# Optimization experiments

Hardware: AMD Instinct MI355X
Metric: run time of the kernel (lower is better)

The kernel has to match this reference:

```python
import jax, jax.numpy as jnp
import numpy as np

N_MESH = 40962  # icosahedral level-6 mesh nodes (x[..., -40962:])


def _lin_coords(out_size, in_size, scale):
    # torch F.interpolate bilinear, align_corners=False source coords
    i = jnp.arange(out_size, dtype=jnp.float32)
    src = jnp.maximum((i + 0.5) / scale - 0.5, 0.0)
    i0 = jnp.clip(jnp.floor(src).astype(jnp.int32), 0, in_size - 1)
    i1 = jnp.minimum(i0 + 1, in_size - 1)
    w = src - i0.astype(jnp.float32)
    return i0, i1, w


def _bilinear4(x):
    # x: (B,C,H,W) -> (B,C,4H,4W), separable bilinear, align_corners=False
    B, C, H, W = x.shape
    i0, i1, wh = _lin_coords(4 * H, H, 4.0)
    x = x[:, :, i0, :] * (1.0 - wh)[None, None, :, None] + x[:, :, i1, :] * wh[None, None, :, None]
    j0, j1, ww = _lin_coords(4 * W, W, 4.0)
    x = x[:, :, :, j0] * (1.0 - ww) + x[:, :, :, j1] * ww
    return x


def _grid2mesh(x, lat, lon):
    # x: (B,C,H,W); drop last lat row, upsample x4, append broadcast pole row
    B, C, H, W = x.shape
    pole = x[:, :, -1, 0][:, :, None, None] * jnp.ones((B, C, 1, 4 * W), x.dtype)
    xi = _bilinear4(x[:, :, :-1, :])            # (B,C,4(H-1),4W)
    xi = jnp.concatenate([xi, pole], axis=2)    # (B,C,4(H-1)+1,4W)
    return xi[:, :, lat - 1, lon - 1]           # (B,C,M) gather at mesh coords


def _gcn(h, W, b, src, dst, norm, n):
    # GCNConv: sym-normalized scatter-add aggregation of linearly transformed feats
    h = h @ W                                    # (B,N,Hd)
    msg = lambda hb: jax.ops.segment_sum(hb[src] * norm[:, None], dst, num_segments=n)
    return jax.vmap(msg)(h) + b


def reference(x, edge_index, Lat, Lon, W1, b1, W2, b2, Wl, bl, Wl1, bl1):
    B, C, H, Wd = x.shape
    mesh = _grid2mesh(x, Lat, Lon)                               # (B,C,M)
    feats = jnp.concatenate([x.reshape(B, C, H * Wd), mesh], -1)  # (B,C,N)
    h = feats.transpose(0, 2, 1)                                 # (B,N,C)
    n = h.shape[1]

    # gcn_norm with self loops (edge_weight = 1)
    loops = jnp.arange(n, dtype=edge_index.dtype)
    src = jnp.concatenate([edge_index[0], loops])
    dst = jnp.concatenate([edge_index[1], loops])
    deg = jax.ops.segment_sum(jnp.ones(src.shape, h.dtype), dst, num_segments=n)
    dinv = jnp.where(deg > 0, deg ** -0.5, 0.0)
    norm = dinv[src] * dinv[dst]

    h = _gcn(h, W1, b1, src, dst, norm, n)
    h = jax.nn.gelu(h, approximate=False)
    h = _gcn(h, W2, b2, src, dst, norm, n)
    h = h[:, -N_MESH:, :]                                        # keep mesh nodes
    out = jax.nn.gelu((h @ Wl + bl) @ Wl1 + bl1, approximate=False)
    return out.transpose(0, 2, 1)                                # (B,out_ch,M)


def setup_inputs() -> dict:
    key = jax.random.key(0)
    ks = jax.random.split(key, 16)
    B, C, H, W = 1, 69, 181, 360
    HID, OUT = 256, 256
    N = H * W + N_MESH  # 106122
    E = 500000
    x = jax.random.normal(ks[0], (B, C, H, W), jnp.float32)
    edge_index = jax.random.randint(ks[1], (2, E), 0, N, dtype=jnp.int64)
    Lat = jax.random.randint(ks[2], (N_MESH,), 1, 4 * (H - 1) + 2, dtype=jnp.int64)
    Lon = jax.random.randint(ks[3], (N_MESH,), 1, 4 * W + 1, dtype=jnp.int64)
    s = 0.05
    return {
        "x": x, "edge_index": edge_index, "Lat": Lat, "Lon": Lon,
        "W1": jax.random.normal(ks[4], (C, HID), jnp.float32) * s,
        "b1": jnp.zeros((HID,), jnp.float32),
        "W2": jax.random.normal(ks[5], (HID, HID), jnp.float32) * s,
        "b2": jnp.zeros((HID,), jnp.float32),
        "Wl": jax.random.normal(ks[6], (HID, 256), jnp.float32) * s,
        "bl": jnp.zeros((256,), jnp.float32),
        "Wl1": jax.random.normal(ks[7], (256, OUT), jnp.float32) * s,
        "bl1": jnp.zeros((OUT,), jnp.float32),
    }
```

## Files before the change

kernel.cpp:

```cpp
#include <hip/hip_runtime.h>

#define NGRID 65160
#define NMESH 40962
#define NTOT  (NGRID + NMESH)
#define CIN   69
#define KPAD1 96
#define HID   256
#define HH    181
#define WWID  360
#define SCAN_BS 1024
#define NBLK_SCAN ((NTOT + SCAN_BS - 1) / SCAN_BS)

#define NT1TILES ((NTOT + 63) / 64)
#define NT1PAD   (NT1TILES * 64)
#define NT2TILES ((NMESH + 63) / 64)
#define NT2PAD   (NT2TILES * 64)

#define W1OFF  0
#define WCOFF  (96 * 256)
#define WALLK  (96 + 256)

typedef float f32x4 __attribute__((ext_vector_type(4)));
typedef _Float16 f16;
typedef _Float16 f16x2 __attribute__((ext_vector_type(2)));
typedef _Float16 f16x4 __attribute__((ext_vector_type(4)));
typedef _Float16 f16x8 __attribute__((ext_vector_type(8)));

__device__ __forceinline__ float gelu_exact(float v) {
    return 0.5f * v * (1.0f + erff(v * 0.7071067811865476f));
}

__global__ __launch_bounds__(256) void transpose_x(const float* __restrict__ x,
                                                   f16* __restrict__ h0g) {
    __shared__ float tile[96][65];
    int s0 = blockIdx.x * 64;
    int t = threadIdx.x;
#pragma unroll
    for (int i = 0; i < 24; ++i) {
        int idx = t + i * 256;
        int c = idx >> 6, s = idx & 63;
        int gs = s0 + s;
        float v = 0.f;
        if (c < CIN && gs < NGRID) v = x[(size_t)c * NGRID + gs];
        tile[c][s] = v;
    }
    __syncthreads();
#pragma unroll
    for (int i = 0; i < 12; ++i) {
        int idx = t + i * 256;
        int r = idx / 48, u = idx % 48;
        int gr = s0 + r;
        if (gr < NGRID) {
            f16x2 p;
            p.x = (f16)tile[u * 2 + 0][r];
            p.y = (f16)tile[u * 2 + 1][r];
            ((f16x2*)h0g)[(size_t)gr * 48 + u] = p;
        }
    }
}

__global__ __launch_bounds__(256) void mesh_interp(const f16* __restrict__ h0g,
                                                   const int* __restrict__ Lat,
                                                   const int* __restrict__ Lon,
                                                   f16* __restrict__ h0m) {
    int t = blockIdx.x * 256 + threadIdx.x;
    if (t >= NMESH * 48) return;
    int j = t / 48, u = t % 48;
    int la = Lat[j] - 1;
    int lo = Lon[j] - 1;
    const f16x2* g = (const f16x2*)h0g;
    f16x2 o;
    if (la == 720) {
        o = g[(size_t)(180 * WWID) * 48 + u];
    } else {
        float sh = fmaxf((la + 0.5f) * 0.25f - 0.5f, 0.0f);
        int i0 = min((int)sh, HH - 2);
        int i1 = min(i0 + 1, HH - 2);
        float wh = sh - (float)i0;
        float sw = fmaxf((lo + 0.5f) * 0.25f - 0.5f, 0.0f);
        int j0 = min((int)sw, WWID - 1);
        int j1 = min(j0 + 1, WWID - 1);
        float ww = sw - (float)j0;
        f16x2 v00 = g[(size_t)(i0 * WWID + j0) * 48 + u];
        f16x2 v10 = g[(size_t)(i1 * WWID + j0) * 48 + u];
        f16x2 v01 = g[(size_t)(i0 * WWID + j1) * 48 + u];
        f16x2 v11 = g[(size_t)(i1 * WWID + j1) * 48 + u];
        float ax = (float)v00.x + ((float)v10.x - (float)v00.x) * wh;
        float ay = (float)v00.y + ((float)v10.y - (float)v00.y) * wh;
        float bx = (float)v01.x + ((float)v11.x - (float)v01.x) * wh;
        float by = (float)v01.y + ((float)v11.y - (float)v01.y) * wh;
        o.x = (f16)(ax + (bx - ax) * ww);
        o.y = (f16)(ay + (by - ay) * ww);
    }
    ((f16x2*)h0m)[(size_t)j * 48 + u] = o;
}

__global__ void deg_init(float* __restrict__ deg, int* __restrict__ cnt) {
    int i = blockIdx.x * 256 + threadIdx.x;
    if (i < NTOT) { deg[i] = 1.0f; cnt[i] = 0; }
}
__global__ void deg_scatter(const int* __restrict__ ei, float* __restrict__ deg, int E) {
    int e = blockIdx.x * 256 + threadIdx.x;
    if (e < E) atomicAdd(&deg[ei[E + e]], 1.0f);
}

__global__ __launch_bounds__(SCAN_BS) void scan1(const float* __restrict__ deg,
                                                 float* __restrict__ dinv,
                                                 int* __restrict__ off, int* __restrict__ bsum) {
    __shared__ int s[SCAN_BS];
    int t = threadIdx.x;
    int i = blockIdx.x * SCAN_BS + t;
    int v = (i < NTOT) ? ((int)deg[i] - 1) : 0;
    if (i < NTOT) dinv[i] = 1.0f / sqrtf((float)(v + 1));
    s[t] = v; __syncthreads();
    for (int d = 1; d < SCAN_BS; d <<= 1) {
        int x = (t >= d) ? s[t - d] : 0;
        __syncthreads();
        s[t] += x;
        __syncthreads();
    }
    if (i < NTOT) off[i] = s[t] - v;
    if (t == SCAN_BS - 1) bsum[blockIdx.x] = s[t];
}
__global__ void scan2(int* __restrict__ bsum) {
    __shared__ int s[128];
    int t = threadIdx.x;
    int v = (t < NBLK_SCAN) ? bsum[t] : 0;
    s[t] = v; __syncthreads();
    for (int d = 1; d < 128; d <<= 1) {
        int x = (t >= d) ? s[t - d] : 0;
        __syncthreads();
        s[t] += x;
        __syncthreads();
    }
    if (t < NBLK_SCAN) bsum[t] = s[t] - v;
}
__global__ __launch_bounds__(SCAN_BS) void scan3(int* __restrict__ off, const int* __restrict__ bsum) {
    int i = blockIdx.x * SCAN_BS + threadIdx.x;
    if (i < NTOT) off[i] += bsum[blockIdx.x];
}

__global__ void csr_fill(const int* __restrict__ ei, const float* __restrict__ dinv,
                         const int* __restrict__ off, int* __restrict__ cnt,
                         int2* __restrict__ epk, int E) {
    int e = blockIdx.x * 256 + threadIdx.x;
    if (e >= E) return;
    int s = ei[e], d = ei[E + e];
    int pos = off[d] + atomicAdd(&cnt[d], 1);
    epk[pos] = make_int2(s, __float_as_int(dinv[s] * dinv[d]));
}

__global__ __launch_bounds__(256) void wgemm(const float* __restrict__ A,
                                             const float* __restrict__ B,
                                             float* __restrict__ C) {
    __shared__ float As[16][68];
    __shared__ float Bs[16][64];
    int r0 = blockIdx.y * 64, c0 = blockIdx.x * 64;
    int t = threadIdx.x;
    int tr = t >> 4, tc = t & 15;
    float acc[4][4] = {};
    for (int kk = 0; kk < 256; kk += 16) {
#pragma unroll
        for (int i = 0; i < 4; ++i) {
            int idx = t + i * 256;
            int r = idx >> 4, k = idx & 15;
            As[k][r] = A[(size_t)(r0 + r) * 256 + kk + k];
        }
#pragma unroll
        for (int i = 0; i < 4; ++i) {
            int idx = t + i * 256;
            int k = idx >> 6, c = idx & 63;
            Bs[k][c] = B[(size_t)(kk + k) * 256 + c0 + c];
        }
        __syncthreads();
#pragma unroll
        for (int k = 0; k < 16; ++k) {
            float a[4], b[4];
#pragma unroll
            for (int i = 0; i < 4; ++i) a[i] = As[k][tr * 4 + i];
#pragma unroll
            for (int j = 0; j < 4; ++j) b[j] = Bs[k][tc * 4 + j];
#pragma unroll
            for (int i = 0; i < 4; ++i)
#pragma unroll
                for (int j = 0; j < 4; ++j) acc[i][j] = fmaf(a[i], b[j], acc[i][j]);
        }
        __syncthreads();
    }
#pragma unroll
    for (int i = 0; i < 4; ++i)
#pragma unroll
        for (int j = 0; j < 4; ++j)
            C[(size_t)(r0 + tr * 4 + i) * 256 + c0 + tc * 4 + j] = acc[i][j];
}

__global__ __launch_bounds__(256) void bias_k(const float* __restrict__ b2,
                                              const float* __restrict__ M1,
                                              const float* __restrict__ bl,
                                              const float* __restrict__ Wl1,
                                              const float* __restrict__ bl1,
                                              float* __restrict__ bc) {
    int c = threadIdx.x;
    float acc = bl1[c];
    for (int j = 0; j < 256; ++j) {
        acc = fmaf(b2[j], M1[(size_t)j * 256 + c], acc);
        acc = fmaf(bl[j], Wl1[(size_t)j * 256 + c], acc);
    }
    bc[c] = acc;
}

__global__ void pack_f16(const float* __restrict__ W1, const float* __restrict__ Wc,
                         f16* __restrict__ wp) {
    int t = blockIdx.x * 256 + threadIdx.x;
    if (t >= WALLK * HID) return;
    int kg = t >> 8, c = t & 255;
    float v;
    size_t idx;
    if (kg < 96) {
        v = (kg < CIN) ? W1[(size_t)kg * HID + c] : 0.f;
        idx = W1OFF + ((((size_t)(kg >> 3)) * HID + c) << 3) + (kg & 7);
    } else {
        int ks = kg - 96;
        int kl = (ks & ~63) + ((ks & 3) << 4) + ((ks & 63) >> 2);
        v = Wc[(size_t)kl * HID + c];
        idx = WCOFF + ((((size_t)(ks >> 3)) * HID + c) << 3) + (ks & 7);
    }
    wp[idx] = (f16)v;
}

__global__ __launch_bounds__(256) void agg1(const f16* __restrict__ h0,
                                            const float* __restrict__ deg,
                                            const float* __restrict__ dinv,
                                            const int* __restrict__ off,
                                            const int2* __restrict__ epk,
                                            f16* __restrict__ P0) {
    int wv = (blockIdx.x * 256 + threadIdx.x) >> 6;
    if (wv >= NT1PAD) return;
    int lane = threadIdx.x & 63;
    if (lane >= 48) return;
    int r = wv & 63, tile = wv >> 6;
    char* dst = (char*)P0 + (size_t)tile * 12288 + ((r * 192 + lane * 4) ^ ((r & 7) << 4));
    if (wv >= NTOT) { *(unsigned*)dst = 0u; return; }
    int d = wv;
    const f16x2* g = (const f16x2*)h0;
    float dv = dinv[d];
    float w2 = dv * dv;
    f16x2 v = g[(size_t)d * 48 + lane];
    float ax = w2 * (float)v.x;
    float ay = w2 * (float)v.y;
    const int2* ep = epk + off[d];
    int n = (int)deg[d] - 1;
    int p = 0;
    for (; p + 4 <= n; p += 4) {
        int2 e0 = ep[p], e1 = ep[p + 1], e2 = ep[p + 2], e3 = ep[p + 3];
        f16x2 u0 = g[(size_t)e0.x * 48 + lane];
        f16x2 u1 = g[(size_t)e1.x * 48 + lane];
        f16x2 u2 = g[(size_t)e2.x * 48 + lane];
        f16x2 u3 = g[(size_t)e3.x * 48 + lane];
        float w0 = __int_as_float(e0.y), w1 = __int_as_float(e1.y);
        float w2b = __int_as_float(e2.y), w3 = __int_as_float(e3.y);
        ax = fmaf(w0, (float)u0.x, ax); ay = fmaf(w0, (float)u0.y, ay);
        ax = fmaf(w1, (float)u1.x, ax); ay = fmaf(w1, (float)u1.y, ay);
        ax = fmaf(w2b, (float)u2.x, ax); ay = fmaf(w2b, (float)u2.y, ay);
        ax = fmaf(w3, (float)u3.x, ax); ay = fmaf(w3, (float)u3.y, ay);
    }
    for (; p < n; ++p) {
        int2 e = ep[p];
        f16x2 u = g[(size_t)e.x * 48 + lane];
        float w = __int_as_float(e.y);
        ax = fmaf(w, (float)u.x, ax);
        ay = fmaf(w, (float)u.y, ay);
    }
    f16x2 o; o.x = (f16)ax; o.y = (f16)ay;
    *(f16x2*)dst = o;
}

__global__ __launch_bounds__(256) void agg2(const f16* __restrict__ A,
                                            const float* __restrict__ deg,
                                            const float* __restrict__ dinv,
                                            const int* __restrict__ off,
                                            const int2* __restrict__ epk,
                                            f16* __restrict__ P2) {
    int wv = (blockIdx.x * 256 + threadIdx.x) >> 6;
    if (wv >= NT2PAD) return;
    int lane = threadIdx.x & 63;
    int r = wv & 63, tile = wv >> 6;
    char* dst = (char*)P2 + (size_t)tile * 32768 + ((r * 512 + lane * 8) ^ ((r & 7) << 4));
    if (wv >= NMESH) { *(unsigned long long*)dst = 0ull; return; }
    int d = NGRID + wv;
    const f16x4* g = (const f16x4*)A;
    float dv = dinv[d];
    float w2 = dv * dv;
    f16x4 v = g[(size_t)d * 64 + lane];
    float4 acc;
    acc.x = w2 * (float)v.x; acc.y = w2 * (float)v.y;
    acc.z = w2 * (float)v.z; acc.w = w2 * (float)v.w;
    const int2* ep = epk + off[d];
    int n = (int)deg[d] - 1;
    int p = 0;
    for (; p + 4 <= n; p += 4) {
        int2 e0 = ep[p], e1 = ep[p + 1], e2 = ep[p + 2], e3 = ep[p + 3];
        f16x4 u0 = g[(size_t)e0.x * 64 + lane];
        f16x4 u1 = g[(size_t)e1.x * 64 + lane];
        f16x4 u2 = g[(size_t)e2.x * 64 + lane];
        f16x4 u3 = g[(size_t)e3.x * 64 + lane];
        float w0 = __int_as_float(e0.y), w1 = __int_as_float(e1.y);
        float w2b = __int_as_float(e2.y), w3 = __int_as_float(e3.y);
        acc.x = fmaf(w0, (float)u0.x, acc.x); acc.y = fmaf(w0, (float)u0.y, acc.y);
        acc.z = fmaf(w0, (float)u0.z, acc.z); acc.w = fmaf(w0, (float)u0.w, acc.w);
        acc.x = fmaf(w1, (float)u1.x, acc.x); acc.y = fmaf(w1, (float)u1.y, acc.y);
        acc.z = fmaf(w1, (float)u1.z, acc.z); acc.w = fmaf(w1, (float)u1.w, acc.w);
        acc.x = fmaf(w2b, (float)u2.x, acc.x); acc.y = fmaf(w2b, (float)u2.y, acc.y);
        acc.z = fmaf(w2b, (float)u2.z, acc.z); acc.w = fmaf(w2b, (float)u2.w, acc.w);
        acc.x = fmaf(w3, (float)u3.x, acc.x); acc.y = fmaf(w3, (float)u3.y, acc.y);
        acc.z = fmaf(w3, (float)u3.z, acc.z); acc.w = fmaf(w3, (float)u3.w, acc.w);
    }
    for (; p < n; ++p) {
        int2 e = ep[p];
        f16x4 u = g[(size_t)e.x * 64 + lane];
        float w = __int_as_float(e.y);
        acc.x = fmaf(w, (float)u.x, acc.x); acc.y = fmaf(w, (float)u.y, acc.y);
        acc.z = fmaf(w, (float)u.z, acc.z); acc.w = fmaf(w, (float)u.w, acc.w);
    }
    f16x4 o;
    o.x = (f16)acc.x; o.y = (f16)acc.y; o.z = (f16)acc.z; o.w = (f16)acc.w;
    *(f16x4*)dst = o;
}

__global__ __launch_bounds__(256) void gemm1_f16(const f16* __restrict__ P0,
                                                 const f16* __restrict__ wp,
                                                 const float* __restrict__ bias,
                                                 f16* __restrict__ Af) {
    __shared__ __align__(16) f16 As[64 * 96];
    const int tile = blockIdx.x;
    const int row0 = tile * 64;
    const int t = threadIdx.x;
    const int lane = t & 63;
    const int wave = t >> 6;
    const int l15 = lane & 15, l4 = lane >> 4;
    const int colw = wave * 64;
    const char* src = (const char*)P0 + (size_t)tile * 12288;
#pragma unroll
    for (int i = 0; i < 3; ++i) {
        int o = t * 16 + i * 4096;
        *(uint4*)((char*)As + o) = *(const uint4*)(src + o);
    }
    __syncthreads();
    f32x4 acc[4][4] = {};
#pragma unroll
    for (int ks = 0; ks < 96; ks += 32) {
        f16x8 a[4], b[4];
#pragma unroll
        for (int rb = 0; rb < 4; ++rb) {
            int r = rb * 16 + l15;
            int byte = r * 192 + (ks + l4 * 8) * 2;
            int swz = byte ^ ((r & 7) << 4);
            a[rb] = *(f16x8*)((char*)As + swz);
        }
#pragma unroll
        for (int cb = 0; cb < 4; ++cb) {
            int c = colw + cb * 16 + l15;
            size_t off = ((((size_t)ks >> 3) + l4) * HID + c) << 3;
            b[cb] = *(const f16x8*)(wp + W1OFF + off);
        }
#pragma unroll
        for (int rb = 0; rb < 4; ++rb)
#pragma unroll
            for (int cb = 0; cb < 4; ++cb)
                acc[rb][cb] = __builtin_amdgcn_mfma_f32_16x16x32_f16(a[rb], b[cb], acc[rb][cb], 0, 0, 0);
    }
#pragma unroll
    for (int rb = 0; rb < 4; ++rb) {
#pragma unroll
        for (int r = 0; r < 4; ++r) {
            int gr = row0 + rb * 16 + l4 * 4 + r;
            if (gr < NTOT) {
                f16x4 o;
#pragma unroll
                for (int cb = 0; cb < 4; ++cb) {
                    int gc = colw + cb * 16 + l15;
                    float v = acc[rb][cb][r] + bias[gc];
                    o[cb] = (f16)gelu_exact(v);
                }
                *(f16x4*)(Af + (size_t)gr * HID + colw + l15 * 4) = o;
            }
        }
    }
}

__global__ __launch_bounds__(256) void final_k(const f16* __restrict__ P2,
                                               const f16* __restrict__ wp,
                                               const float* __restrict__ bc,
                                               float* __restrict__ out) {
    __shared__ __align__(16) char smem[64 * 132 * 4];
    f16* Ps = (f16*)smem;
    float* lf = (float*)smem;
    const int tile = blockIdx.x;
    const int row0 = tile * 64;
    const int t = threadIdx.x;
    const int lane = t & 63;
    const int wave = t >> 6;
    const int l15 = lane & 15, l4 = lane >> 4;
    const int cw = wave * 64;
    const char* src = (const char*)P2 + (size_t)tile * 32768;
#pragma unroll
    for (int i = 0; i < 8; ++i) {
        int o = t * 16 + i * 4096;
        *(uint4*)((char*)Ps + o) = *(const uint4*)(src + o);
    }
    __syncthreads();
    f32x4 acc[4][4] = {};
#pragma unroll
    for (int ks = 0; ks < 256; ks += 32) {
        f16x8 w[4], p[4];
#pragma unroll
        for (int mb = 0; mb < 4; ++mb) {
            int c = cw + mb * 16 + l15;
            size_t off = ((((size_t)ks >> 3) + l4) * HID + c) << 3;
            w[mb] = *(const f16x8*)(wp + WCOFF + off);
        }
#pragma unroll
        for (int jb = 0; jb < 4; ++jb) {
            int r = jb * 16 + l15;
            int byte = r * 512 + (ks + l4 * 8) * 2;
            int swz = byte ^ ((r & 7) << 4);
            p[jb] = *(f16x8*)((char*)Ps + swz);
        }
#pragma unroll
        for (int mb = 0; mb < 4; ++mb)
#pragma unroll
            for (int jb = 0; jb < 4; ++jb)
                acc[mb][jb] = __builtin_amdgcn_mfma_f32_16x16x32_f16(w[mb], p[jb], acc[mb][jb], 0, 0, 0);
    }
    const bool full = (row0 + 64 <= NMESH);
    for (int ph = 0; ph < 2; ++ph) {
        __syncthreads();
        if ((wave >> 1) == ph) {
            int cbase = cw & 127;
#pragma unroll
            for (int mb = 0; mb < 4; ++mb) {
                int chl = cbase + mb * 16 + l4 * 4;
                int c = cw + mb * 16 + l4 * 4;
                float b0 = bc[c + 0], b1v = bc[c + 1], b2v = bc[c + 2], b3v = bc[c + 3];
#pragma unroll
                for (int jb = 0; jb < 4; ++jb) {
                    int j = jb * 16 + l15;
                    float4 o;
                    o.x = gelu_exact(acc[mb][jb][0] + b0);
                    o.y = gelu_exact(acc[mb][jb][1] + b1v);
                    o.z = gelu_exact(acc[mb][jb][2] + b2v);
                    o.w = gelu_exact(acc[mb][jb][3] + b3v);
                    *(float4*)&lf[j * 132 + chl] = o;
                }
            }
        }
        __syncthreads();
        if (full) {
#pragma unroll
            for (int i = 0; i < 8; ++i) {
                int id = t + i * 256;
                int chl = id >> 4, n0 = (id & 15) * 4;
                float4 v;
                v.x = lf[(n0 + 0) * 132 + chl];
                v.y = lf[(n0 + 1) * 132 + chl];
                v.z = lf[(n0 + 2) * 132 + chl];
                v.w = lf[(n0 + 3) * 132 + chl];
                *(float4*)(out + (size_t)(ph * 128 + chl) * NMESH + row0 + n0) = v;
            }
        } else {
            for (int i = 0; i < 8; ++i) {
                int id = t + i * 256;
                int chl = id >> 4, n0 = (id & 15) * 4;
                for (int k2 = 0; k2 < 4; ++k2)
                    if (row0 + n0 + k2 < NMESH)
                        out[(size_t)(ph * 128 + chl) * NMESH + row0 + n0 + k2] =
                            lf[(n0 + k2) * 132 + chl];
            }
        }
    }
}

extern "C" void kernel_launch(void* const* d_in, const int* in_sizes, int n_in,
                              void* d_out, int out_size, void* d_ws, size_t ws_size,
                              hipStream_t stream) {
    const float* x   = (const float*)d_in[0];
    const int*   ei  = (const int*)d_in[1];
    const int*   Lat = (const int*)d_in[2];
    const int*   Lon = (const int*)d_in[3];
    const float* W1  = (const float*)d_in[4];
    const float* b1  = (const float*)d_in[5];
    const float* W2  = (const float*)d_in[6];
    const float* b2  = (const float*)d_in[7];
    const float* Wl  = (const float*)d_in[8];
    const float* bl  = (const float*)d_in[9];
    const float* Wl1 = (const float*)d_in[10];
    const float* bl1 = (const float*)d_in[11];
    float* out = (float*)d_out;
    const int E = in_sizes[1] / 2;

    f16*   h0  = (f16*)d_out;
    int2*  epk = (int2*)((char*)d_out + (size_t)NTOT * KPAD1 * 2);

    f16*   P0   = (f16*)d_ws;
    f16*   Af   = P0 + (size_t)NT1TILES * 6144;
    f16*   P2   = Af + (size_t)NTOT * HID;
    float* deg  = (float*)(P2 + (size_t)NT2TILES * 16384);
    float* dinv = deg + NTOT;
    int*   off  = (int*)(dinv + NTOT);
    int*   cnt  = off + NTOT;
    int*   bsum = cnt + NTOT;
    float* M1   = (float*)(bsum + 128);
    float* WcF  = M1 + HID * HID;
    float* bc   = WcF + HID * HID;
    f16*   wp   = (f16*)(bc + HID);

    transpose_x<<<(NGRID + 63) / 64, 256, 0, stream>>>(x, h0);
    mesh_interp<<<(NMESH * 48 + 255) / 256, 256, 0, stream>>>(h0, Lat, Lon,
                                                              h0 + (size_t)NGRID * KPAD1);

    deg_init<<<(NTOT + 255) / 256, 256, 0, stream>>>(deg, cnt);
    deg_scatter<<<(E + 255) / 256, 256, 0, stream>>>(ei, deg, E);
    scan1<<<NBLK_SCAN, SCAN_BS, 0, stream>>>(deg, dinv, off, bsum);
    scan2<<<1, 128, 0, stream>>>(bsum);
    scan3<<<NBLK_SCAN, SCAN_BS, 0, stream>>>(off, bsum);
    csr_fill<<<(E + 255) / 256, 256, 0, stream>>>(ei, dinv, off, cnt, epk, E);

    dim3 gW(4, 4);
    wgemm<<<gW, 256, 0, stream>>>(Wl, Wl1, M1);
    wgemm<<<gW, 256, 0, stream>>>(W2, M1, WcF);
    bias_k<<<1, 256, 0, stream>>>(b2, M1, bl, Wl1, bl1, bc);
    pack_f16<<<(WALLK * HID + 255) / 256, 256, 0, stream>>>(W1, WcF, wp);

    agg1<<<(int)(((long long)NT1PAD * 64 + 255) / 256), 256, 0, stream>>>(
        h0, deg, dinv, off, epk, P0);
    gemm1_f16<<<NT1TILES, 256, 0, stream>>>(P0, wp, b1, Af);

    agg2<<<(int)(((long long)NT2PAD * 64 + 255) / 256), 256, 0, stream>>>(
        Af, deg, dinv, off, epk, P2);

    final_k<<<NT2TILES, 256, 0, stream>>>(P2, wp, bc, out);
}
```

Baseline: 271.7 us.

## Fuse neighbor aggregation into both GEMM kernels, dropping staged P buffers

The separate agg1/agg2 gather kernels are merged into the MFMA GEMM kernels. Each block now aggregates its 64 rows directly into shared memory, with each wave looping over 16 rows, before running the matmul. This removes the global round-trip of the swizzled P0/P2 intermediates and two kernel launches. The edge list moves from the output buffer to workspace, since fused2 now writes output while other blocks still read edges. The trade-off is far fewer concurrent waves issuing gathers, so there is less latency hiding for the irregular loads.

```diff
diff --git a/kernel.cpp b/kernel.cpp
--- a/kernel.cpp
+++ b/kernel.cpp
@@ -12,9 +12,7 @@
 #define NBLK_SCAN ((NTOT + SCAN_BS - 1) / SCAN_BS)
 
 #define NT1TILES ((NTOT + 63) / 64)
-#define NT1PAD   (NT1TILES * 64)
 #define NT2TILES ((NMESH + 63) / 64)
-#define NT2PAD   (NT2TILES * 64)
 
 #define W1OFF  0
 #define WCOFF  (96 * 256)
@@ -228,109 +226,14 @@
     wp[idx] = (f16)v;
 }
 
-__global__ __launch_bounds__(256) void agg1(const f16* __restrict__ h0,
-                                            const float* __restrict__ deg,
-                                            const float* __restrict__ dinv,
-                                            const int* __restrict__ off,
-                                            const int2* __restrict__ epk,
-                                            f16* __restrict__ P0) {
-    int wv = (blockIdx.x * 256 + threadIdx.x) >> 6;
-    if (wv >= NT1PAD) return;
-    int lane = threadIdx.x & 63;
-    if (lane >= 48) return;
-    int r = wv & 63, tile = wv >> 6;
-    char* dst = (char*)P0 + (size_t)tile * 12288 + ((r * 192 + lane * 4) ^ ((r & 7) << 4));
-    if (wv >= NTOT) { *(unsigned*)dst = 0u; return; }
-    int d = wv;
-    const f16x2* g = (const f16x2*)h0;
-    float dv = dinv[d];
-    float w2 = dv * dv;
-    f16x2 v = g[(size_t)d * 48 + lane];
-    float ax = w2 * (float)v.x;
-    float ay = w2 * (float)v.y;
-    const int2* ep = epk + off[d];
-    int n = (int)deg[d] - 1;
-    int p = 0;
-    for (; p + 4 <= n; p += 4) {
-        int2 e0 = ep[p], e1 = ep[p + 1], e2 = ep[p + 2], e3 = ep[p + 3];
-        f16x2 u0 = g[(size_t)e0.x * 48 + lane];
-        f16x2 u1 = g[(size_t)e1.x * 48 + lane];
-        f16x2 u2 = g[(size_t)e2.x * 48 + lane];
-        f16x2 u3 = g[(size_t)e3.x * 48 + lane];
-        float w0 = __int_as_float(e0.y), w1 = __int_as_float(e1.y);
-        float w2b = __int_as_float(e2.y), w3 = __int_as_float(e3.y);
-        ax = fmaf(w0, (float)u0.x, ax); ay = fmaf(w0, (float)u0.y, ay);
-        ax = fmaf(w1, (float)u1.x, ax); ay = fmaf(w1, (float)u1.y, ay);
-        ax = fmaf(w2b, (float)u2.x, ax); ay = fmaf(w2b, (float)u2.y, ay);
-        ax = fmaf(w3, (float)u3.x, ax); ay = fmaf(w3, (float)u3.y, ay);
-    }
-    for (; p < n; ++p) {
-        int2 e = ep[p];
-        f16x2 u = g[(size_t)e.x * 48 + lane];
-        float w = __int_as_float(e.y);
-        ax = fmaf(w, (float)u.x, ax);
-        ay = fmaf(w, (float)u.y, ay);
-    }
-    f16x2 o; o.x = (f16)ax; o.y = (f16)ay;
-    *(f16x2*)dst = o;
-}
-
-__global__ __launch_bounds__(256) void agg2(const f16* __restrict__ A,
-                                            const float* __restrict__ deg,
-                                            const float* __restrict__ dinv,
-                                            const int* __restrict__ off,
-                                            const int2* __restrict__ epk,
-                                            f16* __restrict__ P2) {
-    int wv = (blockIdx.x * 256 + threadIdx.x) >> 6;
-    if (wv >= NT2PAD) return;
-    int lane = threadIdx.x & 63;
-    int r = wv & 63, tile = wv >> 6;
-    char* dst = (char*)P2 + (size_t)tile * 32768 + ((r * 512 + lane * 8) ^ ((r & 7) << 4));
-    if (wv >= NMESH) { *(unsigned long long*)dst = 0ull; return; }
-    int d = NGRID + wv;
-    const f16x4* g = (const f16x4*)A;
-    float dv = dinv[d];
-    float w2 = dv * dv;
-    f16x4 v = g[(size_t)d * 64 + lane];
-    float4 acc;
-    acc.x = w2 * (float)v.x; acc.y = w2 * (float)v.y;
-    acc.z = w2 * (float)v.z; acc.w = w2 * (float)v.w;
-    const int2* ep = epk + off[d];
-    int n = (int)deg[d] - 1;
-    int p = 0;
-    for (; p + 4 <= n; p += 4) {
-        int2 e0 = ep[p], e1 = ep[p + 1], e2 = ep[p + 2], e3 = ep[p + 3];
-        f16x4 u0 = g[(size_t)e0.x * 64 + lane];
-        f16x4 u1 = g[(size_t)e1.x * 64 + lane];
-        f16x4 u2 = g[(size_t)e2.x * 64 + lane];
-        f16x4 u3 = g[(size_t)e3.x * 64 + lane];
-        float w0 = __int_as_float(e0.y), w1 = __int_as_float(e1.y);
-        float w2b = __int_as_float(e2.y), w3 = __int_as_float(e3.y);
-        acc.x = fmaf(w0, (float)u0.x, acc.x); acc.y = fmaf(w0, (float)u0.y, acc.y);
-        acc.z = fmaf(w0, (float)u0.z, acc.z); acc.w = fmaf(w0, (float)u0.w, acc.w);
-        acc.x = fmaf(w1, (float)u1.x, acc.x); acc.y = fmaf(w1, (float)u1.y, acc.y);
-        acc.z = fmaf(w1, (float)u1.z, acc.z); acc.w = fmaf(w1, (float)u1.w, acc.w);
-        acc.x = fmaf(w2b, (float)u2.x, acc.x); acc.y = fmaf(w2b, (float)u2.y, acc.y);
-        acc.z = fmaf(w2b, (float)u2.z, acc.z); acc.w = fmaf(w2b, (float)u2.w, acc.w);
-        acc.x = fmaf(w3, (float)u3.x, acc.x); acc.y = fmaf(w3, (float)u3.y, acc.y);
-        acc.z = fmaf(w3, (float)u3.z, acc.z); acc.w = fmaf(w3, (float)u3.w, acc.w);
-    }
-    for (; p < n; ++p) {
-        int2 e = ep[p];
-        f16x4 u = g[(size_t)e.x * 64 + lane];
-        float w = __int_as_float(e.y);
-        acc.x = fmaf(w, (float)u.x, acc.x); acc.y = fmaf(w, (float)u.y, acc.y);
-        acc.z = fmaf(w, (float)u.z, acc.z); acc.w = fmaf(w, (float)u.w, acc.w);
-    }
-    f16x4 o;
-    o.x = (f16)acc.x; o.y = (f16)acc.y; o.z = (f16)acc.z; o.w = (f16)acc.w;
-    *(f16x4*)dst = o;
-}
-
-__global__ __launch_bounds__(256) void gemm1_f16(const f16* __restrict__ P0,
-                                                 const f16* __restrict__ wp,
-                                                 const float* __restrict__ bias,
-                                                 f16* __restrict__ Af) {
+__global__ __launch_bounds__(256) void fused1(const f16* __restrict__ h0,
+                                              const float* __restrict__ deg,
+                                              const float* __restrict__ dinv,
+                                              const int* __restrict__ off,
+                                              const int2* __restrict__ epk,
+                                              const f16* __restrict__ wp,
+                                              const float* __restrict__ bias,
+                                              f16* __restrict__ Af) {
     __shared__ __align__(16) f16 As[64 * 96];
     const int tile = blockIdx.x;
     const int row0 = tile * 64;
@@ -339,13 +242,48 @@
     const int wave = t >> 6;
     const int l15 = lane & 15, l4 = lane >> 4;
     const int colw = wave * 64;
-    const char* src = (const char*)P0 + (size_t)tile * 12288;
-#pragma unroll
-    for (int i = 0; i < 3; ++i) {
-        int o = t * 16 + i * 4096;
-        *(uint4*)((char*)As + o) = *(const uint4*)(src + o);
+
+    if (lane < 48) {
+        const f16x2* g = (const f16x2*)h0;
+        for (int i = 0; i < 16; ++i) {
+            int r = wave * 16 + i;
+            int d = row0 + r;
+            char* dst = (char*)As + ((r * 192 + lane * 4) ^ ((r & 7) << 4));
+            if (d >= NTOT) { *(unsigned*)dst = 0u; continue; }
+            float dv = dinv[d];
+            float w2 = dv * dv;
+            f16x2 v = g[(size_t)d * 48 + lane];
+            float ax = w2 * (float)v.x;
+            float ay = w2 * (float)v.y;
+            const int2* ep = epk + off[d];
+            int n = (int)deg[d] - 1;
+            int p = 0;
+            for (; p + 4 <= n; p += 4) {
+                int2 e0 = ep[p], e1 = ep[p + 1], e2 = ep[p + 2], e3 = ep[p + 3];
+                f16x2 u0 = g[(size_t)e0.x * 48 + lane];
+                f16x2 u1 = g[(size_t)e1.x * 48 + lane];
+                f16x2 u2 = g[(size_t)e2.x * 48 + lane];
+                f16x2 u3 = g[(size_t)e3.x * 48 + lane];
+                float w0 = __int_as_float(e0.y), w1 = __int_as_float(e1.y);
+                float w2b = __int_as_float(e2.y), w3 = __int_as_float(e3.y);
+                ax = fmaf(w0, (float)u0.x, ax); ay = fmaf(w0, (float)u0.y, ay);
+                ax = fmaf(w1, (float)u1.x, ax); ay = fmaf(w1, (float)u1.y, ay);
+                ax = fmaf(w2b, (float)u2.x, ax); ay = fmaf(w2b, (float)u2.y, ay);
+                ax = fmaf(w3, (float)u3.x, ax); ay = fmaf(w3, (float)u3.y, ay);
+            }
+            for (; p < n; ++p) {
+                int2 e = ep[p];
+                f16x2 u = g[(size_t)e.x * 48 + lane];
+                float w = __int_as_float(e.y);
+                ax = fmaf(w, (float)u.x, ax);
+                ay = fmaf(w, (float)u.y, ay);
+            }
+            f16x2 o; o.x = (f16)ax; o.y = (f16)ay;
+            *(f16x2*)dst = o;
+        }
     }
     __syncthreads();
+
     f32x4 acc[4][4] = {};
 #pragma unroll
     for (int ks = 0; ks < 96; ks += 32) {
@@ -360,8 +298,8 @@
 #pragma unroll
         for (int cb = 0; cb < 4; ++cb) {
             int c = colw + cb * 16 + l15;
-            size_t off = ((((size_t)ks >> 3) + l4) * HID + c) << 3;
-            b[cb] = *(const f16x8*)(wp + W1OFF + off);
+            size_t o = ((((size_t)ks >> 3) + l4) * HID + c) << 3;
+            b[cb] = *(const f16x8*)(wp + W1OFF + o);
         }
 #pragma unroll
         for (int rb = 0; rb < 4; ++rb)
@@ -388,10 +326,14 @@
     }
 }
 
-__global__ __launch_bounds__(256) void final_k(const f16* __restrict__ P2,
-                                               const f16* __restrict__ wp,
-                                               const float* __restrict__ bc,
-                                               float* __restrict__ out) {
+__global__ __launch_bounds__(256) void fused2(const f16* __restrict__ Af,
+                                              const float* __restrict__ deg,
+                                              const float* __restrict__ dinv,
+                                              const int* __restrict__ off,
+                                              const int2* __restrict__ epk,
+                                              const f16* __restrict__ wp,
+                                              const float* __restrict__ bc,
+                                              float* __restrict__ out) {
     __shared__ __align__(16) char smem[64 * 132 * 4];
     f16* Ps = (f16*)smem;
     float* lf = (float*)smem;
@@ -402,13 +344,55 @@
     const int wave = t >> 6;
     const int l15 = lane & 15, l4 = lane >> 4;
     const int cw = wave * 64;
-    const char* src = (const char*)P2 + (size_t)tile * 32768;
-#pragma unroll
-    for (int i = 0; i < 8; ++i) {
-        int o = t * 16 + i * 4096;
-        *(uint4*)((char*)Ps + o) = *(const uint4*)(src + o);
+
+    {
+        const f16x4* g = (const f16x4*)Af;
+        for (int i = 0; i < 16; ++i) {
+            int r = wave * 16 + i;
+            int j = row0 + r;
+            char* dst = (char*)Ps + ((r * 512 + lane * 8) ^ ((r & 7) << 4));
+            if (j >= NMESH) { *(unsigned long long*)dst = 0ull; continue; }
+            int d = NGRID + j;
+            float dv = dinv[d];
+            float w2 = dv * dv;
+            f16x4 v = g[(size_t)d * 64 + lane];
+            float4 acc;
+            acc.x = w2 * (float)v.x; acc.y = w2 * (float)v.y;
+            acc.z = w2 * (float)v.z; acc.w = w2 * (float)v.w;
+            const int2* ep = epk + off[d];
+            int n = (int)deg[d] - 1;
+            int p = 0;
+            for (; p + 4 <= n; p += 4) {
+                int2 e0 = ep[p], e1 = ep[p + 1], e2 = ep[p + 2], e3 = ep[p + 3];
+                f16x4 u0 = g[(size_t)e0.x * 64 + lane];
+                f16x4 u1 = g[(size_t)e1.x * 64 + lane];
+                f16x4 u2 = g[(size_t)e2.x * 64 + lane];
+                f16x4 u3 = g[(size_t)e3.x * 64 + lane];
+                float w0 = __int_as_float(e0.y), w1 = __int_as_float(e1.y);
+                float w2b = __int_as_float(e2.y), w3 = __int_as_float(e3.y);
+                acc.x = fmaf(w0, (float)u0.x, acc.x); acc.y = fmaf(w0, (float)u0.y, acc.y);
+                acc.z = fmaf(w0, (float)u0.z, acc.z); acc.w = fmaf(w0, (float)u0.w, acc.w);
+                acc.x = fmaf(w1, (float)u1.x, acc.x); acc.y = fmaf(w1, (float)u1.y, acc.y);
+                acc.z = fmaf(w1, (float)u1.z, acc.z); acc.w = fmaf(w1, (float)u1.w, acc.w);
+                acc.x = fmaf(w2b, (float)u2.x, acc.x); acc.y = fmaf(w2b, (float)u2.y, acc.y);
+                acc.z = fmaf(w2b, (float)u2.z, acc.z); acc.w = fmaf(w2b, (float)u2.w, acc.w);
+                acc.x = fmaf(w3, (float)u3.x, acc.x); acc.y = fmaf(w3, (float)u3.y, acc.y);
+                acc.z = fmaf(w3, (float)u3.z, acc.z); acc.w = fmaf(w3, (float)u3.w, acc.w);
+            }
+            for (; p < n; ++p) {
+                int2 e = ep[p];
+                f16x4 u = g[(size_t)e.x * 64 + lane];
+                float w = __int_as_float(e.y);
+                acc.x = fmaf(w, (float)u.x, acc.x); acc.y = fmaf(w, (float)u.y, acc.y);
+                acc.z = fmaf(w, (float)u.z, acc.z); acc.w = fmaf(w, (float)u.w, acc.w);
+            }
+            f16x4 o;
+            o.x = (f16)acc.x; o.y = (f16)acc.y; o.z = (f16)acc.z; o.w = (f16)acc.w;
+            *(f16x4*)dst = o;
+        }
     }
     __syncthreads();
+
     f32x4 acc[4][4] = {};
 #pragma unroll
     for (int ks = 0; ks < 256; ks += 32) {
@@ -416,8 +400,8 @@
 #pragma unroll
         for (int mb = 0; mb < 4; ++mb) {
             int c = cw + mb * 16 + l15;
-            size_t off = ((((size_t)ks >> 3) + l4) * HID + c) << 3;
-            w[mb] = *(const f16x8*)(wp + WCOFF + off);
+            size_t o = ((((size_t)ks >> 3) + l4) * HID + c) << 3;
+            w[mb] = *(const f16x8*)(wp + WCOFF + o);
         }
 #pragma unroll
         for (int jb = 0; jb < 4; ++jb) {
@@ -498,13 +482,11 @@
     float* out = (float*)d_out;
     const int E = in_sizes[1] / 2;
 
-    f16*   h0  = (f16*)d_out;
-    int2*  epk = (int2*)((char*)d_out + (size_t)NTOT * KPAD1 * 2);
-
-    f16*   P0   = (f16*)d_ws;
-    f16*   Af   = P0 + (size_t)NT1TILES * 6144;
-    f16*   P2   = Af + (size_t)NTOT * HID;
-    float* deg  = (float*)(P2 + (size_t)NT2TILES * 16384);
+    f16* h0 = (f16*)d_out;
+
+    f16*   Af   = (f16*)d_ws;
+    int2*  epk  = (int2*)(Af + (size_t)NTOT * HID);
+    float* deg  = (float*)(epk + E);
     float* dinv = deg + NTOT;
     int*   off  = (int*)(dinv + NTOT);
     int*   cnt  = off + NTOT;
@@ -531,12 +513,7 @@
     bias_k<<<1, 256, 0, stream>>>(b2, M1, bl, Wl1, bl1, bc);
     pack_f16<<<(WALLK * HID + 255) / 256, 256, 0, stream>>>(W1, WcF, wp);
 
-    agg1<<<(int)(((long long)NT1PAD * 64 + 255) / 256), 256, 0, stream>>>(
-        h0, deg, dinv, off, epk, P0);
-    gemm1_f16<<<NT1TILES, 256, 0, stream>>>(P0, wp, b1, Af);
-
-    agg2<<<(int)(((long long)NT2PAD * 64 + 255) / 256), 256, 0, stream>>>(
-        Af, deg, dinv, off, epk, P2);
-
-    final_k<<<NT2TILES, 256, 0, stream>>>(P2, wp, bc, out);
-}
+    fused1<<<NT1TILES, 256, 0, stream>>>(h0, deg, dinv, off, epk, wp, b1, Af);
+
+    fused2<<<NT2TILES, 256, 0, stream>>>(Af, deg, dinv, off, epk, wp, bc, out);
+}
```

New measurement: 355.6 us. 1.31x slower.
